# Optimization experiments

Measured on AMD Instinct MI355X. Metric: run time of the kernel, lower is better.

## Reference

```python
import jax, jax.numpy as jnp
import numpy as np

M = 4        # n_memb
D = 8        # n_input + n_control
B = 512      # batch

def setup_inputs() -> dict:
    key = jax.random.key(0)
    input_ = jax.random.uniform(key, (B, M, D), dtype=jnp.float32)
    return {"input_": input_}

def reference(input_):
    # Faithful to RuleLayer.call: for each batch element, take the D columns
    # input_[b, :, d] (each length M) and form their full outer product,
    # flattened so the LAST column varies fastest (matches the matmul chain
    # c[m,...,1] @ xd[1,...,m] followed by reshape).
    b, m, d_tot = input_.shape  # (B, M, D)
    cp = input_[:, :, 0]        # [B, M]
    for d in range(1, d_tot):
        # [B, K, 1] * [B, 1, M] -> [B, K, M] -> [B, K*M]
        cp = (cp[:, :, None] * input_[:, None, :, d]).reshape(b, -1)
    return cp  # [B, M**D]
```

## Files before the change

kernel.cpp:

```cpp
#include <hip/hip_runtime.h>


__global__ __launch_bounds__(256) void rule_outer_kernel(
    const float* __restrict__ in, float* __restrict__ out) {
    const int bb = blockIdx.x;
    const int b = bb >> 2;
    const int q = bb & 3;
    const int t = threadIdx.x;

    __shared__ float x[32];
    __shared__ float head[256];
    __shared__ float tail[256];

    if (t < 32) x[t] = in[b * 32 + t];
    __syncthreads();

    const int j0 = (t >> 6) & 3;
    const int j1 = (t >> 4) & 3;
    const int j2 = (t >> 2) & 3;
    const int j3 = t & 3;
    head[t] = x[j0 * 8 + 0] * x[j1 * 8 + 1] * x[j2 * 8 + 2] * x[j3 * 8 + 3];
    tail[t] = x[j0 * 8 + 4] * x[j1 * 8 + 5] * x[j2 * 8 + 6] * x[j3 * 8 + 7];
    __syncthreads();

    const int lo4 = t & 63;
    const float4 tf = *reinterpret_cast<const float4*>(&tail[lo4 * 4]);
    float4* outv = reinterpret_cast<float4*>(out) + (size_t)b * 16384 + q * 4096;

#pragma unroll
    for (int v = 0; v < 16; ++v) {
        const int f = v * 256 + t;
        const float h = head[(q * 4096 + f) >> 6];
        outv[f] = make_float4(h * tf.x, h * tf.y, h * tf.z, h * tf.w);
    }
}

extern "C" void kernel_launch(void* const* d_in, const int* in_sizes, int n_in,
                              void* d_out, int out_size, void* d_ws, size_t ws_size,
                              hipStream_t stream) {
    const float* in = (const float*)d_in[0];
    float* out = (float*)d_out;
    const int B = in_sizes[0] / 32;
    rule_outer_kernel<<<B * 4, 256, 0, stream>>>(in, out);
}
```

Before: 25.68 us.

## Drop shared-memory staging and use nontemporal vector stores for outer product

Removes the shared-memory head/tail tables and both barriers. Each thread now computes its factor products straight from global input values, which are cached, and regroups the multiplication so each output float4 needs only a small per-iteration product. Output writes use nontemporal stores to avoid polluting the cache for the 32 MB write stream. This adds some redundant global loads and multiplies per thread, and the nontemporal hint may or may not help write bandwidth.

```diff
diff --git a/kernel.cpp b/kernel.cpp
--- a/kernel.cpp
+++ b/kernel.cpp
@@ -1,5 +1,7 @@
 #include <hip/hip_runtime.h>
 
+
+typedef float floatx4 __attribute__((ext_vector_type(4)));
 
 __global__ __launch_bounds__(256) void rule_outer_kernel(
     const float* __restrict__ in, float* __restrict__ out) {
@@ -8,30 +10,24 @@
     const int q = bb & 3;
     const int t = threadIdx.x;
 
-    __shared__ float x[32];
-    __shared__ float head[256];
-    __shared__ float tail[256];
+    const float* xb = in + b * 32;
 
-    if (t < 32) x[t] = in[b * 32 + t];
-    __syncthreads();
+    const float p36 = xb[((t >> 6) & 3) * 8 + 3] * xb[((t >> 4) & 3) * 8 + 4] *
+                      xb[((t >> 2) & 3) * 8 + 5] * xb[(t & 3) * 8 + 6];
+    const float base = xb[q * 8 + 0] * p36;
+    floatx4 tf;
+    tf.x = base * xb[0 * 8 + 7];
+    tf.y = base * xb[1 * 8 + 7];
+    tf.z = base * xb[2 * 8 + 7];
+    tf.w = base * xb[3 * 8 + 7];
 
-    const int j0 = (t >> 6) & 3;
-    const int j1 = (t >> 4) & 3;
-    const int j2 = (t >> 2) & 3;
-    const int j3 = t & 3;
-    head[t] = x[j0 * 8 + 0] * x[j1 * 8 + 1] * x[j2 * 8 + 2] * x[j3 * 8 + 3];
-    tail[t] = x[j0 * 8 + 4] * x[j1 * 8 + 5] * x[j2 * 8 + 6] * x[j3 * 8 + 7];
-    __syncthreads();
-
-    const int lo4 = t & 63;
-    const float4 tf = *reinterpret_cast<const float4*>(&tail[lo4 * 4]);
-    float4* outv = reinterpret_cast<float4*>(out) + (size_t)b * 16384 + q * 4096;
+    floatx4* outv = reinterpret_cast<floatx4*>(out) + (size_t)b * 16384 + q * 4096;
 
 #pragma unroll
     for (int v = 0; v < 16; ++v) {
-        const int f = v * 256 + t;
-        const float h = head[(q * 4096 + f) >> 6];
-        outv[f] = make_float4(h * tf.x, h * tf.y, h * tf.z, h * tf.w);
+        const float h12 = xb[(v >> 2) * 8 + 1] * xb[(v & 3) * 8 + 2];
+        const floatx4 o = h12 * tf;
+        __builtin_nontemporal_store(o, &outv[v * 256 + t]);
     }
 }
 
```

After: 29.50 us. 1.15x slower.
